# Performance work log

Measured on AMD Instinct MI355X. Metric: run time of the kernel, lower is better.

The kernel has to match this reference:

```python
import jax, jax.numpy as jnp
import numpy as np

N, D = 8192, 4096
DIM_K = 4096

def setup_inputs() -> dict:
    key0 = jax.random.key(0)
    k1, k2, k3 = jax.random.split(key0, 3)
    return {
        "query": jax.random.normal(k1, (N, D), dtype=jnp.float32),
        "key": jax.random.normal(k2, (D, N), dtype=jnp.float32),
        "value": jax.random.normal(k3, (N, D), dtype=jnp.float32),
    }

def reference(query, key, value):
    # Faithful to the (buggy) torch module: ELEMENTWISE query * key.T,
    # scale by sqrt(dim_k), elementwise * value, softmax over dim=1
    # (F.softmax's implicit dim for a 2D tensor). The mask branch in the
    # original (`if x:`) cannot execute for multi-element tensors, so it
    # is omitted (mask=None path).
    scale = jnp.sqrt(jnp.float32(DIM_K))
    x = (query * key.T) / scale  # [N, D]
    x = x * value                # [N, D]
    return jax.nn.softmax(x, axis=1)
```

## Files before the change

kernel.cpp:

```cpp
#include <hip/hip_runtime.h>
#include <math.h>


static constexpr int NROW = 8192;
static constexpr int D    = 4096;
static constexpr int RPB  = 8;
static constexpr int HALF = 2048;
static constexpr int LSTR = HALF + 4;
static constexpr int NT   = 16;

#define LDS_BARRIER() asm volatile("s_waitcnt lgkmcnt(0)\n\ts_barrier" ::: "memory")

__global__ __launch_bounds__(512, 4)
void sdp_softmax_kernel(const float* __restrict__ Q,
                        const float* __restrict__ K,
                        const float* __restrict__ V,
                        float* __restrict__ O)
{
    __shared__ float ldsK[RPB * LSTR];

    const int tid  = threadIdx.x;
    const int wv   = tid >> 6;
    const int lane = tid & 63;

    const int nwg = gridDim.x;
    const int cpx = nwg >> 3;
    const int hb  = blockIdx.x;
    const int lb  = (hb & 7) * cpx + (hb >> 3);

    const int row0 = lb * RPB;
    const int r    = row0 + wv;

    const float* qrow = Q + (size_t)r * D;
    const float* vrow = V + (size_t)r * D;
    float*       orow = O + (size_t)r * D;

    const int il = tid & 7;
    const int jg = tid >> 3;
    const float* kbase = K + (size_t)(8 * jg) * NROW + (size_t)row0 + il;
    const float scl = 0.015625f;

    float sa0, sa1, sa2, sa3, sa4, sa5, sa6, sa7;
    float sb0, sb1, sb2, sb3, sb4, sb5, sb6, sb7;
    float sc0, sc1, sc2, sc3, sc4, sc5, sc6, sc7;
    float sd0, sd1, sd2, sd3, sd4, sd5, sd6, sd7;

#define LOADB(R, J0)                                                          \
    {                                                                         \
        const float* p = kbase + (size_t)(J0) * NROW;                         \
        R##0 = p[0];                  R##1 = p[NROW];                         \
        R##2 = p[2 * (size_t)NROW];   R##3 = p[3 * (size_t)NROW];             \
        R##4 = p[4 * (size_t)NROW];   R##5 = p[5 * (size_t)NROW];             \
        R##6 = p[6 * (size_t)NROW];   R##7 = p[7 * (size_t)NROW];             \
    }
#define WRITEB(R, COL)                                                        \
    {                                                                         \
        float* w = &ldsK[il * LSTR + (COL) + 8 * jg];                         \
        *(float4*)w       = make_float4(R##0, R##1, R##2, R##3);              \
        *(float4*)(w + 4) = make_float4(R##4, R##5, R##6, R##7);              \
    }

    LOADB(sa, 0)
    float4 qP0 = *(const float4*)(qrow + 0 * 256 + 4 * lane);
    float4 vP0 = *(const float4*)(vrow + 0 * 256 + 4 * lane);
    float4 qP1 = *(const float4*)(qrow + 1 * 256 + 4 * lane);
    float4 vP1 = *(const float4*)(vrow + 1 * 256 + 4 * lane);
    float4 qP2 = *(const float4*)(qrow + 2 * 256 + 4 * lane);
    float4 vP2 = *(const float4*)(vrow + 2 * 256 + 4 * lane);
    float4 qP3 = *(const float4*)(qrow + 3 * 256 + 4 * lane);
    float4 vP3 = *(const float4*)(vrow + 3 * 256 + 4 * lane);

    LOADB(sb, 512)   WRITEB(sa, 0)
    LOADB(sa, 1024)  WRITEB(sb, 512)
    LOADB(sb, 1536)  WRITEB(sa, 1024)
    WRITEB(sb, 1536)

    LDS_BARRIER();

    float4 e0, e1, e2, e3, e4, e5, e6, e7,
           e8, e9, e10, e11, e12, e13, e14, e15;
    float s = 0.0f;

#define BODY(t, ET, QS, VS)                                                   \
    {                                                                         \
        const float4 qc = QS, vc = VS;                                        \
        if ((t) + 4 < NT) {                                                   \
            QS = *(const float4*)(qrow + ((t) + 4) * 256 + 4 * lane);         \
            VS = *(const float4*)(vrow + ((t) + 4) * 256 + 4 * lane);         \
        }                                                                     \
        const float4 kf =                                                     \
            *(const float4*)&ldsK[wv * LSTR + ((t) & 7) * 256 + 4 * lane];    \
        ET.x = __expf(((qc.x * kf.x) * scl) * vc.x);                          \
        ET.y = __expf(((qc.y * kf.y) * scl) * vc.y);                          \
        ET.z = __expf(((qc.z * kf.z) * scl) * vc.z);                          \
        ET.w = __expf(((qc.w * kf.w) * scl) * vc.w);                          \
        s += ((ET.x + ET.y) + (ET.z + ET.w));                                 \
        __builtin_amdgcn_sched_barrier(0);                                    \
    }

    BODY(0,  e0,  qP0, vP0)
    BODY(1,  e1,  qP1, vP1)
    BODY(2,  e2,  qP2, vP2)
    LOADB(sa, 2048)
    BODY(3,  e3,  qP3, vP3)
    BODY(4,  e4,  qP0, vP0)
    LOADB(sb, 2560)
    BODY(5,  e5,  qP1, vP1)
    BODY(6,  e6,  qP2, vP2)
    LOADB(sc, 3072)
    BODY(7,  e7,  qP3, vP3)
    LOADB(sd, 3584)

    LDS_BARRIER();
    WRITEB(sa, 0)
    WRITEB(sb, 512)
    WRITEB(sc, 1024)
    WRITEB(sd, 1536)
    LDS_BARRIER();

    BODY(8,  e8,  qP0, vP0)
    BODY(9,  e9,  qP1, vP1)
    BODY(10, e10, qP2, vP2)
    BODY(11, e11, qP3, vP3)
    BODY(12, e12, qP0, vP0)
    BODY(13, e13, qP1, vP1)
    BODY(14, e14, qP2, vP2)
    BODY(15, e15, qP3, vP3)
#undef BODY
#undef LOADB
#undef WRITEB

    #pragma unroll
    for (int i = 1; i < 64; i <<= 1)
        s += __shfl_xor(s, i, 64);
    const float inv = 1.0f / s;

#define WRITE_TILE(t, ET)                                                     \
    {                                                                         \
        float4 xx = ET;                                                       \
        xx.x *= inv; xx.y *= inv; xx.z *= inv; xx.w *= inv;                   \
        *(float4*)(orow + (size_t)(t) * 256 + 4 * lane) = xx;                 \
    }

    WRITE_TILE(0,  e0)  WRITE_TILE(1,  e1)  WRITE_TILE(2,  e2)  WRITE_TILE(3,  e3)
    WRITE_TILE(4,  e4)  WRITE_TILE(5,  e5)  WRITE_TILE(6,  e6)  WRITE_TILE(7,  e7)
    WRITE_TILE(8,  e8)  WRITE_TILE(9,  e9)  WRITE_TILE(10, e10) WRITE_TILE(11, e11)
    WRITE_TILE(12, e12) WRITE_TILE(13, e13) WRITE_TILE(14, e14) WRITE_TILE(15, e15)
#undef WRITE_TILE
}

extern "C" void kernel_launch(void* const* d_in, const int* in_sizes, int n_in,
                              void* d_out, int out_size, void* d_ws, size_t ws_size,
                              hipStream_t stream) {
    const float* Q = (const float*)d_in[0];
    const float* K = (const float*)d_in[1];
    const float* V = (const float*)d_in[2];
    float* O = (float*)d_out;

    dim3 grid(NROW / RPB);
    dim3 block(512);
    sdp_softmax_kernel<<<grid, block, 0, stream>>>(Q, K, V, O);
}
```

Measured before the change: 127.6 us.

## Pre-transpose K into workspace and stream contiguous rows in main kernel

Adds a tiled LDS transpose kernel that writes K^T into the workspace buffer, then a simpler streaming kernel reads contiguous rows of Q, K^T and V with coalesced float4 loads. This aims to remove the strided column reads and LDS staging of K in the fused kernel. It adds an extra full read and write of K through memory plus a second launch. The old kernel stays as a fallback when the workspace is too small.

```diff
diff --git a/kernel.cpp b/kernel.cpp
--- a/kernel.cpp
+++ b/kernel.cpp
@@ -4,31 +4,152 @@
 
 static constexpr int NROW = 8192;
 static constexpr int D    = 4096;
-static constexpr int RPB  = 8;
-static constexpr int HALF = 2048;
-static constexpr int LSTR = HALF + 4;
-static constexpr int NT   = 16;
-
-#define LDS_BARRIER() asm volatile("s_waitcnt lgkmcnt(0)\n\ts_barrier" ::: "memory")
-
-__global__ __launch_bounds__(512, 4)
-void sdp_softmax_kernel(const float* __restrict__ Q,
-                        const float* __restrict__ K,
-                        const float* __restrict__ V,
-                        float* __restrict__ O)
+static constexpr float SCL = 0.015625f;
+
+__global__ __launch_bounds__(256, 2)
+void kt_transpose_kernel(const float* __restrict__ K, float* __restrict__ KT)
 {
-    __shared__ float ldsK[RPB * LSTR];
-
+    __shared__ float lds[64][257];
+    const int t  = threadIdx.x;
+    const int jt = blockIdx.x & 63;
+    const int it = blockIdx.x >> 6;
+    const int j0 = jt * 64;
+    const int i0 = it * 256;
+
+    const int rr = t >> 6;
+    const int i4 = t & 63;
+    #pragma unroll
+    for (int s = 0; s < 16; ++s) {
+        const int jr = s * 4 + rr;
+        const float4 v =
+            *(const float4*)(K + (size_t)(j0 + jr) * NROW + i0 + 4 * i4);
+        *(float4*)&lds[jr][4 * i4] = v;
+    }
+    __syncthreads();
+
+    const int j4 = t & 15;
+    const int ir = t >> 4;
+    #pragma unroll
+    for (int sw = 0; sw < 16; ++sw) {
+        const int il = sw * 16 + ir;
+        float4 w;
+        w.x = lds[4 * j4 + 0][il];
+        w.y = lds[4 * j4 + 1][il];
+        w.z = lds[4 * j4 + 2][il];
+        w.w = lds[4 * j4 + 3][il];
+        *(float4*)(KT + (size_t)(i0 + il) * D + j0 + 4 * j4) = w;
+    }
+}
+
+__global__ __launch_bounds__(256, 3)
+void sdp_stream_kernel(const float* __restrict__ Q,
+                       const float* __restrict__ KT,
+                       const float* __restrict__ V,
+                       float* __restrict__ O)
+{
     const int tid  = threadIdx.x;
     const int wv   = tid >> 6;
     const int lane = tid & 63;
-
+    const int r    = blockIdx.x * 4 + wv;
+
+    const float* qrow = Q  + (size_t)r * D;
+    const float* krow = KT + (size_t)r * D;
+    const float* vrow = V  + (size_t)r * D;
+    float*       orow = O  + (size_t)r * D;
+    const int c0 = 4 * lane;
+
+    float4 qA = *(const float4*)(qrow + 0 * 256 + c0);
+    float4 kA = *(const float4*)(krow + 0 * 256 + c0);
+    float4 vA = *(const float4*)(vrow + 0 * 256 + c0);
+    float4 qB = *(const float4*)(qrow + 1 * 256 + c0);
+    float4 kB = *(const float4*)(krow + 1 * 256 + c0);
+    float4 vB = *(const float4*)(vrow + 1 * 256 + c0);
+    float4 qC = *(const float4*)(qrow + 2 * 256 + c0);
+    float4 kC = *(const float4*)(krow + 2 * 256 + c0);
+    float4 vC = *(const float4*)(vrow + 2 * 256 + c0);
+    float4 qD = *(const float4*)(qrow + 3 * 256 + c0);
+    float4 kD = *(const float4*)(krow + 3 * 256 + c0);
+    float4 vD = *(const float4*)(vrow + 3 * 256 + c0);
+
+    float4 e0, e1, e2, e3, e4, e5, e6, e7,
+           e8, e9, e10, e11, e12, e13, e14, e15;
+    float s = 0.0f;
+
+#define BODY(t, ET, QS, KS, VS)                                               \
+    {                                                                         \
+        const float4 qc = QS, kc = KS, vc = VS;                               \
+        if ((t) + 4 < 16) {                                                   \
+            QS = *(const float4*)(qrow + ((t) + 4) * 256 + c0);               \
+            KS = *(const float4*)(krow + ((t) + 4) * 256 + c0);               \
+            VS = *(const float4*)(vrow + ((t) + 4) * 256 + c0);               \
+        }                                                                     \
+        ET.x = __expf(((qc.x * kc.x) * SCL) * vc.x);                          \
+        ET.y = __expf(((qc.y * kc.y) * SCL) * vc.y);                          \
+        ET.z = __expf(((qc.z * kc.z) * SCL) * vc.z);                          \
+        ET.w = __expf(((qc.w * kc.w) * SCL) * vc.w);                          \
+        s += ((ET.x + ET.y) + (ET.z + ET.w));                                 \
+        __builtin_amdgcn_sched_barrier(0);                                    \
+    }
+
+    BODY(0,  e0,  qA, kA, vA)
+    BODY(1,  e1,  qB, kB, vB)
+    BODY(2,  e2,  qC, kC, vC)
+    BODY(3,  e3,  qD, kD, vD)
+    BODY(4,  e4,  qA, kA, vA)
+    BODY(5,  e5,  qB, kB, vB)
+    BODY(6,  e6,  qC, kC, vC)
+    BODY(7,  e7,  qD, kD, vD)
+    BODY(8,  e8,  qA, kA, vA)
+    BODY(9,  e9,  qB, kB, vB)
+    BODY(10, e10, qC, kC, vC)
+    BODY(11, e11, qD, kD, vD)
+    BODY(12, e12, qA, kA, vA)
+    BODY(13, e13, qB, kB, vB)
+    BODY(14, e14, qC, kC, vC)
+    BODY(15, e15, qD, kD, vD)
+#undef BODY
+
+    #pragma unroll
+    for (int i = 1; i < 64; i <<= 1)
+        s += __shfl_xor(s, i, 64);
+    const float inv = 1.0f / s;
+
+#define WRITE_TILE(t, ET)                                                     \
+    {                                                                         \
+        float4 xx = ET;                                                       \
+        xx.x *= inv; xx.y *= inv; xx.z *= inv; xx.w *= inv;                   \
+        *(float4*)(orow + (size_t)(t) * 256 + c0) = xx;                       \
+    }
+
+    WRITE_TILE(0,  e0)  WRITE_TILE(1,  e1)  WRITE_TILE(2,  e2)  WRITE_TILE(3,  e3)
+    WRITE_TILE(4,  e4)  WRITE_TILE(5,  e5)  WRITE_TILE(6,  e6)  WRITE_TILE(7,  e7)
+    WRITE_TILE(8,  e8)  WRITE_TILE(9,  e9)  WRITE_TILE(10, e10) WRITE_TILE(11, e11)
+    WRITE_TILE(12, e12) WRITE_TILE(13, e13) WRITE_TILE(14, e14) WRITE_TILE(15, e15)
+#undef WRITE_TILE
+}
+
+static constexpr int RPB_F  = 8;
+static constexpr int HALF_F = 2048;
+static constexpr int LSTR_F = HALF_F + 4;
+
+#define LDS_BARRIER() asm volatile("s_waitcnt lgkmcnt(0)\n\ts_barrier" ::: "memory")
+
+__global__ __launch_bounds__(512, 4)
+void sdp_softmax_fallback(const float* __restrict__ Q,
+                          const float* __restrict__ K,
+                          const float* __restrict__ V,
+                          float* __restrict__ O)
+{
+    __shared__ float ldsK[RPB_F * LSTR_F];
+
+    const int tid  = threadIdx.x;
+    const int wv   = tid >> 6;
+    const int lane = tid & 63;
     const int nwg = gridDim.x;
     const int cpx = nwg >> 3;
     const int hb  = blockIdx.x;
     const int lb  = (hb & 7) * cpx + (hb >> 3);
-
-    const int row0 = lb * RPB;
+    const int row0 = lb * RPB_F;
     const int r    = row0 + wv;
 
     const float* qrow = Q + (size_t)r * D;
@@ -38,7 +159,6 @@
     const int il = tid & 7;
     const int jg = tid >> 3;
     const float* kbase = K + (size_t)(8 * jg) * NROW + (size_t)row0 + il;
-    const float scl = 0.015625f;
 
     float sa0, sa1, sa2, sa3, sa4, sa5, sa6, sa7;
     float sb0, sb1, sb2, sb3, sb4, sb5, sb6, sb7;
@@ -55,7 +175,7 @@
     }
 #define WRITEB(R, COL)                                                        \
     {                                                                         \
-        float* w = &ldsK[il * LSTR + (COL) + 8 * jg];                         \
+        float* w = &ldsK[il * LSTR_F + (COL) + 8 * jg];                       \
         *(float4*)w       = make_float4(R##0, R##1, R##2, R##3);              \
         *(float4*)(w + 4) = make_float4(R##4, R##5, R##6, R##7);              \
     }
@@ -84,16 +204,16 @@
 #define BODY(t, ET, QS, VS)                                                   \
     {                                                                         \
         const float4 qc = QS, vc = VS;                                        \
-        if ((t) + 4 < NT) {                                                   \
+        if ((t) + 4 < 16) {                                                   \
             QS = *(const float4*)(qrow + ((t) + 4) * 256 + 4 * lane);         \
             VS = *(const float4*)(vrow + ((t) + 4) * 256 + 4 * lane);         \
         }                                                                     \
         const float4 kf =                                                     \
-            *(const float4*)&ldsK[wv * LSTR + ((t) & 7) * 256 + 4 * lane];    \
-        ET.x = __expf(((qc.x * kf.x) * scl) * vc.x);                          \
-        ET.y = __expf(((qc.y * kf.y) * scl) * vc.y);                          \
-        ET.z = __expf(((qc.z * kf.z) * scl) * vc.z);                          \
-        ET.w = __expf(((qc.w * kf.w) * scl) * vc.w);                          \
+            *(const float4*)&ldsK[wv * LSTR_F + ((t) & 7) * 256 + 4 * lane];  \
+        ET.x = __expf(((qc.x * kf.x) * SCL) * vc.x);                          \
+        ET.y = __expf(((qc.y * kf.y) * SCL) * vc.y);                          \
+        ET.z = __expf(((qc.z * kf.z) * SCL) * vc.z);                          \
+        ET.w = __expf(((qc.w * kf.w) * SCL) * vc.w);                          \
         s += ((ET.x + ET.y) + (ET.z + ET.w));                                 \
         __builtin_amdgcn_sched_barrier(0);                                    \
     }
@@ -157,7 +277,12 @@
     const float* V = (const float*)d_in[2];
     float* O = (float*)d_out;
 
-    dim3 grid(NROW / RPB);
-    dim3 block(512);
-    sdp_softmax_kernel<<<grid, block, 0, stream>>>(Q, K, V, O);
-}
+    const size_t kt_bytes = (size_t)NROW * D * sizeof(float);
+    if (ws_size >= kt_bytes) {
+        float* KT = (float*)d_ws;
+        kt_transpose_kernel<<<dim3(64 * 32), dim3(256), 0, stream>>>(K, KT);
+        sdp_stream_kernel<<<dim3(NROW / 4), dim3(256), 0, stream>>>(Q, KT, V, O);
+    } else {
+        sdp_softmax_fallback<<<dim3(NROW / RPB_F), dim3(512), 0, stream>>>(Q, K, V, O);
+    }
+}
```

Result: slower. 170.1 us (+33.3%).
